# Optimization experiments

Hardware: AMD Instinct MI355X
Metric: run time of the kernel (lower is better)

Reference implementation:

```python
import jax, jax.numpy as jnp
import numpy as np

B, L, D, H, N = 1, 768, 128, 8, 6  # batch, seq len, model dim, heads, core_num
DH = D // H
EPS = 1e-5


def _layernorm(x, g, b):
    m = jnp.mean(x, axis=-1, keepdims=True)
    v = jnp.mean(jnp.square(x - m), axis=-1, keepdims=True)
    return (x - m) * jax.lax.rsqrt(v + EPS) * g + b


def setup_inputs() -> dict:
    key = jax.random.key(0)
    ks = jax.random.split(key, 12)
    s = 0.05

    def w(k, shape):
        return jax.random.normal(k, shape, dtype=jnp.float32) * s

    return {
        "x": jax.random.normal(ks[0], (B, L, D), dtype=jnp.float32),
        # JCrossOutProduct: l (in->mid), lo (mid->out); torch Linear convention y = x @ W.T + b
        "cop_l_w": w(ks[1], (N, D, D)), "cop_l_b": jnp.zeros((N, D), jnp.float32),
        "cop_lo_w": w(ks[2], (N, D, D)), "cop_lo_b": jnp.zeros((N, D), jnp.float32),
        # JResCOPAttn.l
        "cop_out_w": w(ks[3], (N, D, D)), "cop_out_b": jnp.zeros((N, D), jnp.float32),
        "cop_ln_g": jnp.ones((N, D), jnp.float32), "cop_ln_b": jnp.zeros((N, D), jnp.float32),
        # nn.MultiheadAttention: packed qkv in_proj + out_proj
        "qkv_w": w(ks[4], (N, 3 * D, D)), "qkv_b": jnp.zeros((N, 3 * D), jnp.float32),
        "mha_out_w": w(ks[5], (N, D, D)), "mha_out_b": jnp.zeros((N, D), jnp.float32),
        "mha_ln_g": jnp.ones((N, D), jnp.float32), "mha_ln_b": jnp.zeros((N, D), jnp.float32),
        # final l1
        "l1_w": w(ks[6], (D, D)), "l1_b": jnp.zeros((D,), jnp.float32),
    }


def reference(x, cop_l_w, cop_l_b, cop_lo_w, cop_lo_b, cop_out_w, cop_out_b,
              cop_ln_g, cop_ln_b, qkv_w, qkv_b, mha_out_w, mha_out_b,
              mha_ln_g, mha_ln_b, l1_w, l1_b):
    scale = 1.0 / np.sqrt(DH)
    for i in range(N):
        # ---- JResCOPAttn branch (AlphaFold-style outer product mean) ----
        a = x @ cop_l_w[i].T + cop_l_b[i]                          # [B,L,D]
        tm = jnp.einsum('bic,bjc->bijc', a, a)                     # [B,L,L,D] outer product
        tm = jnp.einsum('bijc,oc->bijo', tm, cop_lo_w[i]) + cop_lo_b[i]
        tx = x @ cop_out_w[i].T + cop_out_b[i]                     # [B,L,D]
        y1 = x + jnp.einsum('bijo,bjo->bio', tm, tx)               # '...cab,...ab->...cb'
        x1 = _layernorm(y1, cop_ln_g[i], cop_ln_b[i])              # dropout/act are identity
        # ---- JResSelfAttn branch (standard MHA, batch_first) ----
        qkv = x @ qkv_w[i].T + qkv_b[i]                            # [B,L,3D]
        q, k, v = jnp.split(qkv, 3, axis=-1)
        q = q.reshape(B, L, H, DH)
        k = k.reshape(B, L, H, DH)
        v = v.reshape(B, L, H, DH)
        scores = jnp.einsum('bihd,bjhd->bhij', q, k) * scale       # [B,H,L,L]
        attn = jax.nn.softmax(scores, axis=-1)
        o = jnp.einsum('bhij,bjhd->bihd', attn, v).reshape(B, L, D)
        y2 = x + (o @ mha_out_w[i].T + mha_out_b[i])
        x2 = _layernorm(y2, mha_ln_g[i], mha_ln_b[i])
        # ---- combine ----
        x = x + x1 + x2
    return x @ l1_w.T + l1_b
```

## Files before the change

kernel.cpp:

```cpp
#include <hip/hip_runtime.h>

#define L_SEQ 768
#define P_SZ  (L_SEQ * 128)

__device__ __forceinline__ unsigned short f2bf(float x) {
    unsigned int u = __float_as_uint(x);
    unsigned int r = (u + 0x7fffu + ((u >> 16) & 1u)) >> 16;
    return (unsigned short)r;
}

__device__ __forceinline__ void stage_x_tile(int tid, int r0, bool first,
    bool writeback, const float* xprev, const float* y1, const float* y2,
    const float* g1, const float* b1, const float* g2, const float* b2,
    float* xcur, float (*As)[132])
{
    const int row = tid >> 3;
    const int cs  = (tid & 7) * 16;
    const int gr  = (r0 + row) * 128 + cs;
    if (first) {
#pragma unroll
        for (int u = 0; u < 4; ++u)
            *(float4*)&As[row][cs + 4 * u] = *(const float4*)&xprev[gr + 4 * u];
        return;
    }
    float4 v1[4], v2[4];
    float s1 = 0.0f, s2 = 0.0f;
#pragma unroll
    for (int u = 0; u < 4; ++u) {
        v1[u] = *(const float4*)&y1[gr + 4 * u];
        v2[u] = *(const float4*)&y2[gr + 4 * u];
        s1 += v1[u].x + v1[u].y + v1[u].z + v1[u].w;
        s2 += v2[u].x + v2[u].y + v2[u].z + v2[u].w;
    }
#pragma unroll
    for (int m = 1; m < 8; m <<= 1) { s1 += __shfl_xor(s1, m); s2 += __shfl_xor(s2, m); }
    const float mu1 = s1 * (1.0f / 128.0f), mu2 = s2 * (1.0f / 128.0f);
    float q1 = 0.0f, q2 = 0.0f;
#pragma unroll
    for (int u = 0; u < 4; ++u) {
        float d;
        d = v1[u].x - mu1; q1 += d * d;  d = v1[u].y - mu1; q1 += d * d;
        d = v1[u].z - mu1; q1 += d * d;  d = v1[u].w - mu1; q1 += d * d;
        d = v2[u].x - mu2; q2 += d * d;  d = v2[u].y - mu2; q2 += d * d;
        d = v2[u].z - mu2; q2 += d * d;  d = v2[u].w - mu2; q2 += d * d;
    }
#pragma unroll
    for (int m = 1; m < 8; m <<= 1) { q1 += __shfl_xor(q1, m); q2 += __shfl_xor(q2, m); }
    const float rs1 = rsqrtf(q1 * (1.0f / 128.0f) + 1e-5f);
    const float rs2 = rsqrtf(q2 * (1.0f / 128.0f) + 1e-5f);
#pragma unroll
    for (int u = 0; u < 4; ++u) {
        float4 ga = *(const float4*)&g1[cs + 4 * u];
        float4 ba = *(const float4*)&b1[cs + 4 * u];
        float4 gb = *(const float4*)&g2[cs + 4 * u];
        float4 bb = *(const float4*)&b2[cs + 4 * u];
        float4 xv = *(const float4*)&xprev[gr + 4 * u];
        float4 o;
        o.x = xv.x + (v1[u].x - mu1) * rs1 * ga.x + ba.x + (v2[u].x - mu2) * rs2 * gb.x + bb.x;
        o.y = xv.y + (v1[u].y - mu1) * rs1 * ga.y + ba.y + (v2[u].y - mu2) * rs2 * gb.y + bb.y;
        o.z = xv.z + (v1[u].z - mu1) * rs1 * ga.z + ba.z + (v2[u].z - mu2) * rs2 * gb.z + bb.z;
        o.w = xv.w + (v1[u].w - mu1) * rs1 * ga.w + ba.w + (v2[u].w - mu2) * rs2 * gb.w + bb.w;
        *(float4*)&As[row][cs + 4 * u] = o;
        if (writeback) *(float4*)&xcur[gr + 4 * u] = o;
    }
}

__global__ __launch_bounds__(256) void megaK(int first,
    const float* __restrict__ xprev, const float* __restrict__ y1,
    const float* __restrict__ y2, float* __restrict__ xcur,
    const float* __restrict__ g1, const float* __restrict__ b1,
    const float* __restrict__ g2, const float* __restrict__ b2,
    const float* __restrict__ lw, const float* __restrict__ lb,
    const float* __restrict__ ow, const float* __restrict__ ob,
    const float* __restrict__ qw, const float* __restrict__ qb,
    float* __restrict__ a, float* __restrict__ tx, float* __restrict__ qkv)
{
    __shared__ float Bs[64][132];
    __shared__ float As[32][132];
    const int bid = blockIdx.x;
    const int tid = threadIdx.x;
    const int ct = bid / 24, rt = bid % 24;
    const int r0 = rt * 32;
    stage_x_tile(tid, r0, first != 0, (!first && ct == 0), xprev, y1, y2,
                 g1, b1, g2, b2, xcur, As);
    const float* W; const float* bias; float* outp; int ldC, colbase;
    if (ct < 2)      { W = lw; bias = lb; outp = a;   ldC = 128; colbase = ct * 64; }
    else if (ct < 4) { W = ow; bias = ob; outp = tx;  ldC = 128; colbase = (ct - 2) * 64; }
    else             { W = qw; bias = qb; outp = qkv; ldC = 384; colbase = (ct - 4) * 64; }
#pragma unroll
    for (int t = 0; t < 8; ++t) {
        int idx = tid + 256 * t;
        int brow = idx >> 5, f4 = idx & 31;
        *(float4*)&Bs[brow][f4 * 4] = *(const float4*)&W[(colbase + brow) * 128 + f4 * 4];
    }
    __syncthreads();
    const int rg = tid >> 4, ng = tid & 15;
    float accs[2][4];
#pragma unroll
    for (int c = 0; c < 4; ++c) {
        float bv = bias[colbase + ng + 16 * c];
        accs[0][c] = bv; accs[1][c] = bv;
    }
#pragma unroll 8
    for (int kk = 0; kk < 32; ++kk) {
        float4 a1 = *(const float4*)&As[rg][kk * 4];
        float4 a2 = *(const float4*)&As[rg + 16][kk * 4];
#pragma unroll
        for (int c = 0; c < 4; ++c) {
            float4 b = *(const float4*)&Bs[ng + 16 * c][kk * 4];
            accs[0][c] += a1.x * b.x + a1.y * b.y + a1.z * b.z + a1.w * b.w;
            accs[1][c] += a2.x * b.x + a2.y * b.y + a2.z * b.z + a2.w * b.w;
        }
    }
    const int r1 = r0 + rg, r2 = r0 + rg + 16;
#pragma unroll
    for (int c = 0; c < 4; ++c) {
        int gc = colbase + ng + 16 * c;
        outp[r1 * ldC + gc] = accs[0][c];
        outp[r2 * ldC + gc] = accs[1][c];
    }
}

__global__ __launch_bounds__(256) void k2K(const float* __restrict__ qkv,
    const float* __restrict__ a_, const float* __restrict__ tx_,
    float* __restrict__ o_, float* __restrict__ Mpart, float* __restrict__ tspart)
{
    __shared__ __align__(16) char smem[61440];
    const int bid = blockIdx.x;
    const int tid = threadIdx.x;
    if (bid < 192) {
        float* Ks = (float*)smem;
        float* Vs = Ks + 384 * 20;
        const int h = bid / 24;
        const int ch = bid % 24;
        const int base = ch * 32;
        const int lane = tid & 63;
        const int w = tid >> 6;
        const int p = lane & 31;
        const int rgidx = w * 2 + (lane >> 5);

        float q[4][16];
#pragma unroll
        for (int rr = 0; rr < 4; ++rr) {
            int r = base + rgidx * 4 + rr;
            const float4* qr = (const float4*)(qkv + r * 384 + h * 16);
#pragma unroll
            for (int s = 0; s < 4; ++s) {
                float4 v = qr[s];
                q[rr][s * 4 + 0] = v.x; q[rr][s * 4 + 1] = v.y;
                q[rr][s * 4 + 2] = v.z; q[rr][s * 4 + 3] = v.w;
            }
        }
        float m[4], l[4], acc[4][16];
#pragma unroll
        for (int rr = 0; rr < 4; ++rr) {
            m[rr] = -1e30f; l[rr] = 0.0f;
#pragma unroll
            for (int d = 0; d < 16; ++d) acc[rr][d] = 0.0f;
        }
        for (int ps = 0; ps < 2; ++ps) {
            __syncthreads();
#pragma unroll
            for (int t = 0; t < 6; ++t) {
                int idx = tid + 256 * t;
                int jj = idx >> 2, seg = idx & 3;
                int j = ps * 384 + jj;
                *(float4*)&Ks[jj * 20 + seg * 4] =
                    *(const float4*)&qkv[j * 384 + 128 + h * 16 + seg * 4];
                *(float4*)&Vs[jj * 20 + seg * 4] =
                    *(const float4*)&qkv[j * 384 + 256 + h * 16 + seg * 4];
            }
            __syncthreads();
            for (int jj2 = 0; jj2 < 12; ++jj2) {
                int jl = jj2 * 32 + p;
                float k16[16], v16[16];
#pragma unroll
                for (int s = 0; s < 4; ++s) {
                    float4 kv = *(const float4*)&Ks[jl * 20 + s * 4];
                    k16[s * 4 + 0] = kv.x; k16[s * 4 + 1] = kv.y;
                    k16[s * 4 + 2] = kv.z; k16[s * 4 + 3] = kv.w;
                    float4 vv = *(const float4*)&Vs[jl * 20 + s * 4];
                    v16[s * 4 + 0] = vv.x; v16[s * 4 + 1] = vv.y;
                    v16[s * 4 + 2] = vv.z; v16[s * 4 + 3] = vv.w;
                }
#pragma unroll
                for (int rr = 0; rr < 4; ++rr) {
                    float sc = 0.0f;
#pragma unroll
                    for (int d = 0; d < 16; ++d) sc += q[rr][d] * k16[d];
                    sc *= 0.25f;
                    if (sc > m[rr] + 8.0f) {
                        float f = __expf(m[rr] - sc);
                        l[rr] *= f;
#pragma unroll
                        for (int d = 0; d < 16; ++d) acc[rr][d] *= f;
                        m[rr] = sc;
                    }
                    float pe = __expf(sc - m[rr]);
                    l[rr] += pe;
#pragma unroll
                    for (int d = 0; d < 16; ++d) acc[rr][d] += pe * v16[d];
                }
            }
        }
        __syncthreads();
        float* sm = (float*)smem;
        float* sl = sm + 1024;
        unsigned short* sacc = (unsigned short*)(sl + 1024);
#pragma unroll
        for (int rr = 0; rr < 4; ++rr) {
            int row = rgidx * 4 + rr;
            sm[p * 32 + row] = m[rr];
            sl[p * 32 + row] = l[rr];
            unsigned int wbuf[8];
#pragma unroll
            for (int d2 = 0; d2 < 8; ++d2) {
                unsigned int lo = f2bf(acc[rr][2 * d2]);
                unsigned int hi = f2bf(acc[rr][2 * d2 + 1]);
                wbuf[d2] = lo | (hi << 16);
            }
            uint4* dst = (uint4*)&sacc[(p * 32 + row) * 24];
            dst[0] = make_uint4(wbuf[0], wbuf[1], wbuf[2], wbuf[3]);
            dst[1] = make_uint4(wbuf[4], wbuf[5], wbuf[6], wbuf[7]);
        }
        __syncthreads();
        {
            const int row = tid >> 3, dp = tid & 7;
            float M = -1e30f;
#pragma unroll
            for (int pp = 0; pp < 32; ++pp) M = fmaxf(M, sm[pp * 32 + row]);
            float L = 0.0f, o0 = 0.0f, o1 = 0.0f;
#pragma unroll
            for (int pp = 0; pp < 32; ++pp) {
                float f = __expf(sm[pp * 32 + row] - M);
                L += sl[pp * 32 + row] * f;
                unsigned int wv = *(const unsigned int*)&sacc[(pp * 32 + row) * 24 + 2 * dp];
                o0 += f * __uint_as_float(wv << 16);
                o1 += f * __uint_as_float(wv & 0xffff0000u);
            }
            float inv = 1.0f / L;
            *(float2*)&o_[(base + row) * 128 + h * 16 + 2 * dp] =
                make_float2(o0 * inv, o1 * inv);
        }
    } else {
        const int idx0 = bid - 192;
        const int jc = idx0 >> 2, ot = idx0 & 3;
        const int j0 = jc * 48;
        float* As  = (float*)smem;
        float* Ts  = As + 48 * 128;
        float* red = Ts + 48 * 32;
#pragma unroll
        for (int t = 0; t < 6; ++t) {
            int ix = tid + 256 * t;
            int jj = ix >> 5, f4 = ix & 31;
            *(float4*)&As[jj * 128 + f4 * 4] =
                *(const float4*)&a_[(j0 + jj) * 128 + f4 * 4];
        }
#pragma unroll
        for (int t = 0; t < 2; ++t) {
            int ix = tid + 256 * t;
            if (ix < 384) {
                int jj = ix >> 3, f4 = ix & 7;
                *(float4*)&Ts[jj * 32 + f4 * 4] =
                    *(const float4*)&tx_[(j0 + jj) * 128 + ot * 32 + f4 * 4];
            }
        }
        __syncthreads();
        const int c4 = tid & 31, owt = tid >> 5;
        float accm[4][4] = {};
#pragma unroll 4
        for (int jj = 0; jj < 48; ++jj) {
            float4 av = *(const float4*)&As[jj * 128 + c4 * 4];
            float4 tv = *(const float4*)&Ts[jj * 32 + owt * 4];
            float avv[4] = {av.x, av.y, av.z, av.w};
            float tvv[4] = {tv.x, tv.y, tv.z, tv.w};
#pragma unroll
            for (int oi = 0; oi < 4; ++oi)
#pragma unroll
                for (int ci = 0; ci < 4; ++ci)
                    accm[oi][ci] += avv[ci] * tvv[oi];
        }
#pragma unroll
        for (int oi = 0; oi < 4; ++oi) {
            *(float4*)&Mpart[jc * 16384 + (ot * 32 + owt * 4 + oi) * 128 + c4 * 4] =
                make_float4(accm[oi][0], accm[oi][1], accm[oi][2], accm[oi][3]);
        }
        {
            const int o = tid & 31, g = tid >> 5;
            float s = 0.0f;
#pragma unroll
            for (int jj = 0; jj < 6; ++jj) s += Ts[(g * 6 + jj) * 32 + o];
            red[g * 32 + o] = s;
        }
        __syncthreads();
        if (tid < 32) {
            float s = 0.0f;
#pragma unroll
            for (int g = 0; g < 8; ++g) s += red[g * 32 + tid];
            tspart[jc * 128 + ot * 32 + tid] = s;
        }
    }
}

__global__ __launch_bounds__(256) void ygemmK(
    const float* __restrict__ a_, const float* __restrict__ o_,
    const float* __restrict__ Mpart, const float* __restrict__ lo_w,
    const float* __restrict__ lob, const float* __restrict__ tspart,
    const float* __restrict__ mw, const float* __restrict__ mb,
    const float* __restrict__ xc, float* __restrict__ y1, float* __restrict__ y2)
{
    __shared__ float Bs[64][132];
    const int bid = blockIdx.x;
    const int tid = threadIdx.x;
    const int yb = bid / 24, rt = bid % 24;
    const float* A; float* C; int colbase;
    if (yb < 2) {
        colbase = yb * 64; A = a_; C = y1;
#pragma unroll
        for (int t = 0; t < 8; ++t) {
            int idx = tid + 256 * t;
            int row = idx >> 5, f4 = idx & 31;
            int o = colbase + row;
            float4 s = make_float4(0.f, 0.f, 0.f, 0.f);
#pragma unroll
            for (int jc = 0; jc < 16; ++jc) {
                float4 mv = *(const float4*)&Mpart[jc * 16384 + o * 128 + f4 * 4];
                s.x += mv.x; s.y += mv.y; s.z += mv.z; s.w += mv.w;
            }
            float4 lw4 = *(const float4*)&lo_w[o * 128 + f4 * 4];
            s.x *= lw4.x; s.y *= lw4.y; s.z *= lw4.z; s.w *= lw4.w;
            *(float4*)&Bs[row][f4 * 4] = s;
        }
    } else {
        colbase = (yb - 2) * 64; A = o_; C = y2;
#pragma unroll
        for (int t = 0; t < 8; ++t) {
            int idx = tid + 256 * t;
            int row = idx >> 5, f4 = idx & 31;
            *(float4*)&Bs[row][f4 * 4] =
                *(const float4*)&mw[(colbase + row) * 128 + f4 * 4];
        }
    }
    __syncthreads();
    const int rg = tid >> 4, ng = tid & 15;
    const int r0 = rt * 32;
    const int r1 = r0 + rg, r2 = r0 + rg + 16;
    float accs[2][4];
#pragma unroll
    for (int c = 0; c < 4; ++c) {
        int gc = colbase + ng + 16 * c;
        float bv;
        if (yb < 2) {
            float s = 0.0f;
#pragma unroll
            for (int jc = 0; jc < 16; ++jc) s += tspart[jc * 128 + gc];
            bv = lob[gc] * s;
        } else {
            bv = mb[gc];
        }
        accs[0][c] = bv; accs[1][c] = bv;
    }
    const float* A1 = A + r1 * 128;
    const float* A2 = A + r2 * 128;
#pragma unroll 8
    for (int kk = 0; kk < 32; ++kk) {
        float4 a1 = *(const float4*)&A1[kk * 4];
        float4 a2 = *(const float4*)&A2[kk * 4];
#pragma unroll
        for (int c = 0; c < 4; ++c) {
            float4 b = *(const float4*)&Bs[ng + 16 * c][kk * 4];
            accs[0][c] += a1.x * b.x + a1.y * b.y + a1.z * b.z + a1.w * b.w;
            accs[1][c] += a2.x * b.x + a2.y * b.y + a2.z * b.z + a2.w * b.w;
        }
    }
#pragma unroll
    for (int c = 0; c < 4; ++c) {
        int gc = colbase + ng + 16 * c;
        C[r1 * 128 + gc] = xc[r1 * 128 + gc] + accs[0][c];
        C[r2 * 128 + gc] = xc[r2 * 128 + gc] + accs[1][c];
    }
}

__global__ __launch_bounds__(256) void finK(
    const float* __restrict__ xprev, const float* __restrict__ y1,
    const float* __restrict__ y2,
    const float* __restrict__ g1, const float* __restrict__ b1,
    const float* __restrict__ g2, const float* __restrict__ b2,
    const float* __restrict__ w, const float* __restrict__ bias,
    float* __restrict__ outp)
{
    __shared__ float Bs[64][132];
    __shared__ float As[32][132];
    const int bid = blockIdx.x;
    const int tid = threadIdx.x;
    const int ct = bid / 24, rt = bid % 24;
    const int r0 = rt * 32;
    const int colbase = ct * 64;
    stage_x_tile(tid, r0, false, false, xprev, y1, y2, g1, b1, g2, b2,
                 nullptr, As);
#pragma unroll
    for (int t = 0; t < 8; ++t) {
        int idx = tid + 256 * t;
        int brow = idx >> 5, f4 = idx & 31;
        *(float4*)&Bs[brow][f4 * 4] = *(const float4*)&w[(colbase + brow) * 128 + f4 * 4];
    }
    __syncthreads();
    const int rg = tid >> 4, ng = tid & 15;
    float accs[2][4];
#pragma unroll
    for (int c = 0; c < 4; ++c) {
        float bv = bias[colbase + ng + 16 * c];
        accs[0][c] = bv; accs[1][c] = bv;
    }
#pragma unroll 8
    for (int kk = 0; kk < 32; ++kk) {
        float4 a1 = *(const float4*)&As[rg][kk * 4];
        float4 a2 = *(const float4*)&As[rg + 16][kk * 4];
#pragma unroll
        for (int c = 0; c < 4; ++c) {
            float4 b = *(const float4*)&Bs[ng + 16 * c][kk * 4];
            accs[0][c] += a1.x * b.x + a1.y * b.y + a1.z * b.z + a1.w * b.w;
            accs[1][c] += a2.x * b.x + a2.y * b.y + a2.z * b.z + a2.w * b.w;
        }
    }
    const int r1 = r0 + rg, r2 = r0 + rg + 16;
#pragma unroll
    for (int c = 0; c < 4; ++c) {
        int gc = colbase + ng + 16 * c;
        outp[r1 * 128 + gc] = accs[0][c];
        outp[r2 * 128 + gc] = accs[1][c];
    }
}

extern "C" void kernel_launch(void* const* d_in, const int* in_sizes, int n_in,
                              void* d_out, int out_size, void* d_ws, size_t ws_size,
                              hipStream_t stream)
{
    const float* x_in      = (const float*)d_in[0];
    const float* cop_l_w   = (const float*)d_in[1];
    const float* cop_l_b   = (const float*)d_in[2];
    const float* cop_lo_w  = (const float*)d_in[3];
    const float* cop_lo_b  = (const float*)d_in[4];
    const float* cop_out_w = (const float*)d_in[5];
    const float* cop_out_b = (const float*)d_in[6];
    const float* cop_ln_g  = (const float*)d_in[7];
    const float* cop_ln_b  = (const float*)d_in[8];
    const float* qkv_w     = (const float*)d_in[9];
    const float* qkv_b     = (const float*)d_in[10];
    const float* mha_out_w = (const float*)d_in[11];
    const float* mha_out_b = (const float*)d_in[12];
    const float* mha_ln_g  = (const float*)d_in[13];
    const float* mha_ln_b  = (const float*)d_in[14];
    const float* l1_w      = (const float*)d_in[15];
    const float* l1_b      = (const float*)d_in[16];

    float* ws = (float*)d_ws;
    float* xA     = ws + 0 * P_SZ;
    float* xB     = ws + 1 * P_SZ;
    float* a_     = ws + 2 * P_SZ;
    float* tx_    = ws + 3 * P_SZ;
    float* y1_    = ws + 4 * P_SZ;
    float* y2_    = ws + 5 * P_SZ;
    float* qkv_   = ws + 6 * P_SZ;
    float* o_     = ws + 9 * P_SZ;
    float* Mpart  = ws + 10 * P_SZ;
    float* tspart = Mpart + 16 * 16384;

    const float* xc = x_in;

    for (int i = 0; i < 6; ++i) {
        const float* lw  = cop_l_w   + i * 16384;
        const float* lb  = cop_l_b   + i * 128;
        const float* low = cop_lo_w  + i * 16384;
        const float* lob = cop_lo_b  + i * 128;
        const float* ow  = cop_out_w + i * 16384;
        const float* ob  = cop_out_b + i * 128;
        const float* qw  = qkv_w     + i * 49152;
        const float* qb  = qkv_b     + i * 384;
        const float* mw  = mha_out_w + i * 16384;
        const float* mb  = mha_out_b + i * 128;
        const float* pg1 = cop_ln_g + (i - 1) * 128;
        const float* pb1 = cop_ln_b + (i - 1) * 128;
        const float* pg2 = mha_ln_g + (i - 1) * 128;
        const float* pb2 = mha_ln_b + (i - 1) * 128;

        if (i == 0) {
            megaK<<<240, 256, 0, stream>>>(1, x_in, nullptr, nullptr, nullptr,
                                           nullptr, nullptr, nullptr, nullptr,
                                           lw, lb, ow, ob, qw, qb, a_, tx_, qkv_);
        } else {
            float* xn = (i & 1) ? xB : xA;
            megaK<<<240, 256, 0, stream>>>(0, xc, y1_, y2_, xn,
                                           pg1, pb1, pg2, pb2,
                                           lw, lb, ow, ob, qw, qb, a_, tx_, qkv_);
            xc = xn;
        }
        k2K<<<256, 256, 0, stream>>>(qkv_, a_, tx_, o_, Mpart, tspart);
        ygemmK<<<96, 256, 0, stream>>>(a_, o_, Mpart, low, lob, tspart, mw, mb,
                                       xc, y1_, y2_);
    }

    finK<<<48, 256, 0, stream>>>(xc, y1_, y2_,
                                 cop_ln_g + 5 * 128, cop_ln_b + 5 * 128,
                                 mha_ln_g + 5 * 128, mha_ln_b + 5 * 128,
                                 l1_w, l1_b, (float*)d_out);
}
```

Before: 284.4 us.

## Halve row tiles and restructure attention to raise block counts across kernels

Shrinks the row tile of the GEMM-style kernels (megaK, ygemmK, finK) from 32 to 16 rows, doubling grid sizes. The attention part of k2K is reworked so each thread handles one query row over a 12-key slice, with 16 partial softmax states merged through fp32 shared memory instead of bf16. The outer-product partial reduction now loops over two 48-row halves per block, halving the number of Mpart partials. The aim is more blocks and occupancy on a small problem, at the cost of less register reuse per thread and fewer keys processed per thread in attention.

```diff
diff --git a/kernel.cpp b/kernel.cpp
--- a/kernel.cpp
+++ b/kernel.cpp
@@ -3,41 +3,35 @@
 #define L_SEQ 768
 #define P_SZ  (L_SEQ * 128)
 
-__device__ __forceinline__ unsigned short f2bf(float x) {
-    unsigned int u = __float_as_uint(x);
-    unsigned int r = (u + 0x7fffu + ((u >> 16) & 1u)) >> 16;
-    return (unsigned short)r;
-}
-
-__device__ __forceinline__ void stage_x_tile(int tid, int r0, bool first,
+__device__ __forceinline__ void stage16(int tid, int r0, bool first,
     bool writeback, const float* xprev, const float* y1, const float* y2,
     const float* g1, const float* b1, const float* g2, const float* b2,
     float* xcur, float (*As)[132])
 {
-    const int row = tid >> 3;
-    const int cs  = (tid & 7) * 16;
+    const int row = tid >> 4;
+    const int cs  = (tid & 15) * 8;
     const int gr  = (r0 + row) * 128 + cs;
     if (first) {
 #pragma unroll
-        for (int u = 0; u < 4; ++u)
+        for (int u = 0; u < 2; ++u)
             *(float4*)&As[row][cs + 4 * u] = *(const float4*)&xprev[gr + 4 * u];
         return;
     }
-    float4 v1[4], v2[4];
+    float4 v1[2], v2[2];
     float s1 = 0.0f, s2 = 0.0f;
 #pragma unroll
-    for (int u = 0; u < 4; ++u) {
+    for (int u = 0; u < 2; ++u) {
         v1[u] = *(const float4*)&y1[gr + 4 * u];
         v2[u] = *(const float4*)&y2[gr + 4 * u];
         s1 += v1[u].x + v1[u].y + v1[u].z + v1[u].w;
         s2 += v2[u].x + v2[u].y + v2[u].z + v2[u].w;
     }
 #pragma unroll
-    for (int m = 1; m < 8; m <<= 1) { s1 += __shfl_xor(s1, m); s2 += __shfl_xor(s2, m); }
+    for (int m = 1; m < 16; m <<= 1) { s1 += __shfl_xor(s1, m); s2 += __shfl_xor(s2, m); }
     const float mu1 = s1 * (1.0f / 128.0f), mu2 = s2 * (1.0f / 128.0f);
     float q1 = 0.0f, q2 = 0.0f;
 #pragma unroll
-    for (int u = 0; u < 4; ++u) {
+    for (int u = 0; u < 2; ++u) {
         float d;
         d = v1[u].x - mu1; q1 += d * d;  d = v1[u].y - mu1; q1 += d * d;
         d = v1[u].z - mu1; q1 += d * d;  d = v1[u].w - mu1; q1 += d * d;
@@ -45,11 +39,11 @@
         d = v2[u].z - mu2; q2 += d * d;  d = v2[u].w - mu2; q2 += d * d;
     }
 #pragma unroll
-    for (int m = 1; m < 8; m <<= 1) { q1 += __shfl_xor(q1, m); q2 += __shfl_xor(q2, m); }
+    for (int m = 1; m < 16; m <<= 1) { q1 += __shfl_xor(q1, m); q2 += __shfl_xor(q2, m); }
     const float rs1 = rsqrtf(q1 * (1.0f / 128.0f) + 1e-5f);
     const float rs2 = rsqrtf(q2 * (1.0f / 128.0f) + 1e-5f);
 #pragma unroll
-    for (int u = 0; u < 4; ++u) {
+    for (int u = 0; u < 2; ++u) {
         float4 ga = *(const float4*)&g1[cs + 4 * u];
         float4 ba = *(const float4*)&b1[cs + 4 * u];
         float4 gb = *(const float4*)&g2[cs + 4 * u];
@@ -65,7 +59,7 @@
     }
 }
 
-__global__ __launch_bounds__(256) void megaK(int first,
+__global__ __launch_bounds__(256, 4) void megaK(int first,
     const float* __restrict__ xprev, const float* __restrict__ y1,
     const float* __restrict__ y2, float* __restrict__ xcur,
     const float* __restrict__ g1, const float* __restrict__ b1,
@@ -76,13 +70,13 @@
     float* __restrict__ a, float* __restrict__ tx, float* __restrict__ qkv)
 {
     __shared__ float Bs[64][132];
-    __shared__ float As[32][132];
+    __shared__ float As[16][132];
     const int bid = blockIdx.x;
     const int tid = threadIdx.x;
-    const int ct = bid / 24, rt = bid % 24;
-    const int r0 = rt * 32;
-    stage_x_tile(tid, r0, first != 0, (!first && ct == 0), xprev, y1, y2,
-                 g1, b1, g2, b2, xcur, As);
+    const int ct = bid / 48, rt = bid % 48;
+    const int r0 = rt * 16;
+    stage16(tid, r0, first != 0, (!first && ct == 0), xprev, y1, y2,
+            g1, b1, g2, b2, xcur, As);
     const float* W; const float* bias; float* outp; int ldC, colbase;
     if (ct < 2)      { W = lw; bias = lb; outp = a;   ldC = 128; colbase = ct * 64; }
     else if (ct < 4) { W = ow; bias = ob; outp = tx;  ldC = 128; colbase = (ct - 2) * 64; }
@@ -95,202 +89,170 @@
     }
     __syncthreads();
     const int rg = tid >> 4, ng = tid & 15;
-    float accs[2][4];
-#pragma unroll
-    for (int c = 0; c < 4; ++c) {
-        float bv = bias[colbase + ng + 16 * c];
-        accs[0][c] = bv; accs[1][c] = bv;
-    }
+    float accs[4];
+#pragma unroll
+    for (int c = 0; c < 4; ++c) accs[c] = bias[colbase + ng + 16 * c];
 #pragma unroll 8
     for (int kk = 0; kk < 32; ++kk) {
         float4 a1 = *(const float4*)&As[rg][kk * 4];
-        float4 a2 = *(const float4*)&As[rg + 16][kk * 4];
 #pragma unroll
         for (int c = 0; c < 4; ++c) {
             float4 b = *(const float4*)&Bs[ng + 16 * c][kk * 4];
-            accs[0][c] += a1.x * b.x + a1.y * b.y + a1.z * b.z + a1.w * b.w;
-            accs[1][c] += a2.x * b.x + a2.y * b.y + a2.z * b.z + a2.w * b.w;
-        }
-    }
-    const int r1 = r0 + rg, r2 = r0 + rg + 16;
-#pragma unroll
-    for (int c = 0; c < 4; ++c) {
-        int gc = colbase + ng + 16 * c;
-        outp[r1 * ldC + gc] = accs[0][c];
-        outp[r2 * ldC + gc] = accs[1][c];
-    }
-}
-
-__global__ __launch_bounds__(256) void k2K(const float* __restrict__ qkv,
+            accs[c] += a1.x * b.x + a1.y * b.y + a1.z * b.z + a1.w * b.w;
+        }
+    }
+    const int r = r0 + rg;
+#pragma unroll
+    for (int c = 0; c < 4; ++c)
+        outp[r * ldC + colbase + ng + 16 * c] = accs[c];
+}
+
+__global__ __launch_bounds__(256, 4) void k2K(const float* __restrict__ qkv,
     const float* __restrict__ a_, const float* __restrict__ tx_,
     float* __restrict__ o_, float* __restrict__ Mpart, float* __restrict__ tspart)
 {
-    __shared__ __align__(16) char smem[61440];
+    __shared__ __align__(16) char smem[49152];
     const int bid = blockIdx.x;
     const int tid = threadIdx.x;
-    if (bid < 192) {
+    if (bid < 384) {
         float* Ks = (float*)smem;
-        float* Vs = Ks + 384 * 20;
-        const int h = bid / 24;
-        const int ch = bid % 24;
-        const int base = ch * 32;
-        const int lane = tid & 63;
-        const int w = tid >> 6;
-        const int p = lane & 31;
-        const int rgidx = w * 2 + (lane >> 5);
-
-        float q[4][16];
-#pragma unroll
-        for (int rr = 0; rr < 4; ++rr) {
-            int r = base + rgidx * 4 + rr;
-            const float4* qr = (const float4*)(qkv + r * 384 + h * 16);
+        float* Vs = Ks + 192 * 20;
+        float* sm = Vs + 192 * 20;
+        float* sl = sm + 256;
+        float* sacc = sl + 256;
+        const int h = bid / 48;
+        const int ch = bid % 48;
+        const int r = tid & 15;
+        const int part = tid >> 4;
+        const int qi = ch * 16 + r;
+
+        float q[16];
+        {
+            const float4* qr = (const float4*)(qkv + qi * 384 + h * 16);
 #pragma unroll
             for (int s = 0; s < 4; ++s) {
                 float4 v = qr[s];
-                q[rr][s * 4 + 0] = v.x; q[rr][s * 4 + 1] = v.y;
-                q[rr][s * 4 + 2] = v.z; q[rr][s * 4 + 3] = v.w;
-            }
-        }
-        float m[4], l[4], acc[4][16];
-#pragma unroll
-        for (int rr = 0; rr < 4; ++rr) {
-            m[rr] = -1e30f; l[rr] = 0.0f;
-#pragma unroll
-            for (int d = 0; d < 16; ++d) acc[rr][d] = 0.0f;
-        }
-        for (int ps = 0; ps < 2; ++ps) {
+                q[s * 4 + 0] = v.x; q[s * 4 + 1] = v.y;
+                q[s * 4 + 2] = v.z; q[s * 4 + 3] = v.w;
+            }
+        }
+        float m = -1e30f, l = 0.0f;
+        float acc[16];
+#pragma unroll
+        for (int d = 0; d < 16; ++d) acc[d] = 0.0f;
+
+        for (int s = 0; s < 4; ++s) {
             __syncthreads();
 #pragma unroll
-            for (int t = 0; t < 6; ++t) {
+            for (int t = 0; t < 3; ++t) {
                 int idx = tid + 256 * t;
-                int jj = idx >> 2, seg = idx & 3;
-                int j = ps * 384 + jj;
-                *(float4*)&Ks[jj * 20 + seg * 4] =
-                    *(const float4*)&qkv[j * 384 + 128 + h * 16 + seg * 4];
-                *(float4*)&Vs[jj * 20 + seg * 4] =
-                    *(const float4*)&qkv[j * 384 + 256 + h * 16 + seg * 4];
+                int row = idx >> 2, d4 = idx & 3;
+                int j = s * 192 + row;
+                *(float4*)&Ks[row * 20 + d4 * 4] =
+                    *(const float4*)&qkv[j * 384 + 128 + h * 16 + d4 * 4];
+                *(float4*)&Vs[row * 20 + d4 * 4] =
+                    *(const float4*)&qkv[j * 384 + 256 + h * 16 + d4 * 4];
             }
             __syncthreads();
-            for (int jj2 = 0; jj2 < 12; ++jj2) {
-                int jl = jj2 * 32 + p;
-                float k16[16], v16[16];
-#pragma unroll
-                for (int s = 0; s < 4; ++s) {
-                    float4 kv = *(const float4*)&Ks[jl * 20 + s * 4];
-                    k16[s * 4 + 0] = kv.x; k16[s * 4 + 1] = kv.y;
-                    k16[s * 4 + 2] = kv.z; k16[s * 4 + 3] = kv.w;
-                    float4 vv = *(const float4*)&Vs[jl * 20 + s * 4];
-                    v16[s * 4 + 0] = vv.x; v16[s * 4 + 1] = vv.y;
-                    v16[s * 4 + 2] = vv.z; v16[s * 4 + 3] = vv.w;
+            const int tb = part * 12;
+            for (int jj = 0; jj < 12; ++jj) {
+                int t = tb + jj;
+                float sc = 0.0f;
+#pragma unroll
+                for (int d = 0; d < 16; ++d) sc += q[d] * Ks[t * 20 + d];
+                sc *= 0.25f;
+                float p;
+                if (sc > m) {
+                    float f = __expf(m - sc);
+                    l *= f;
+#pragma unroll
+                    for (int d = 0; d < 16; ++d) acc[d] *= f;
+                    m = sc;
+                    p = 1.0f;
+                } else {
+                    p = __expf(sc - m);
                 }
-#pragma unroll
-                for (int rr = 0; rr < 4; ++rr) {
-                    float sc = 0.0f;
-#pragma unroll
-                    for (int d = 0; d < 16; ++d) sc += q[rr][d] * k16[d];
-                    sc *= 0.25f;
-                    if (sc > m[rr] + 8.0f) {
-                        float f = __expf(m[rr] - sc);
-                        l[rr] *= f;
-#pragma unroll
-                        for (int d = 0; d < 16; ++d) acc[rr][d] *= f;
-                        m[rr] = sc;
-                    }
-                    float pe = __expf(sc - m[rr]);
-                    l[rr] += pe;
-#pragma unroll
-                    for (int d = 0; d < 16; ++d) acc[rr][d] += pe * v16[d];
-                }
-            }
-        }
+                l += p;
+#pragma unroll
+                for (int d = 0; d < 16; ++d) acc[d] += p * Vs[t * 20 + d];
+            }
+        }
+        sm[part * 16 + r] = m;
+        sl[part * 16 + r] = l;
+#pragma unroll
+        for (int d = 0; d < 16; ++d) sacc[(part * 16 + r) * 16 + d] = acc[d];
         __syncthreads();
-        float* sm = (float*)smem;
-        float* sl = sm + 1024;
-        unsigned short* sacc = (unsigned short*)(sl + 1024);
-#pragma unroll
-        for (int rr = 0; rr < 4; ++rr) {
-            int row = rgidx * 4 + rr;
-            sm[p * 32 + row] = m[rr];
-            sl[p * 32 + row] = l[rr];
-            unsigned int wbuf[8];
-#pragma unroll
-            for (int d2 = 0; d2 < 8; ++d2) {
-                unsigned int lo = f2bf(acc[rr][2 * d2]);
-                unsigned int hi = f2bf(acc[rr][2 * d2 + 1]);
-                wbuf[d2] = lo | (hi << 16);
-            }
-            uint4* dst = (uint4*)&sacc[(p * 32 + row) * 24];
-            dst[0] = make_uint4(wbuf[0], wbuf[1], wbuf[2], wbuf[3]);
-            dst[1] = make_uint4(wbuf[4], wbuf[5], wbuf[6], wbuf[7]);
-        }
-        __syncthreads();
-        {
-            const int row = tid >> 3, dp = tid & 7;
-            float M = -1e30f;
-#pragma unroll
-            for (int pp = 0; pp < 32; ++pp) M = fmaxf(M, sm[pp * 32 + row]);
-            float L = 0.0f, o0 = 0.0f, o1 = 0.0f;
-#pragma unroll
-            for (int pp = 0; pp < 32; ++pp) {
-                float f = __expf(sm[pp * 32 + row] - M);
-                L += sl[pp * 32 + row] * f;
-                unsigned int wv = *(const unsigned int*)&sacc[(pp * 32 + row) * 24 + 2 * dp];
-                o0 += f * __uint_as_float(wv << 16);
-                o1 += f * __uint_as_float(wv & 0xffff0000u);
-            }
-            float inv = 1.0f / L;
-            *(float2*)&o_[(base + row) * 128 + h * 16 + 2 * dp] =
-                make_float2(o0 * inv, o1 * inv);
-        }
+
+        const int row = tid >> 4, d = tid & 15;
+        float M = sm[row];
+#pragma unroll
+        for (int p = 1; p < 16; ++p) M = fmaxf(M, sm[p * 16 + row]);
+        float L = 0.0f, o = 0.0f;
+#pragma unroll
+        for (int p = 0; p < 16; ++p) {
+            float f = __expf(sm[p * 16 + row] - M);
+            L += sl[p * 16 + row] * f;
+            o += sacc[(p * 16 + row) * 16 + d] * f;
+        }
+        o_[(ch * 16 + row) * 128 + h * 16 + d] = o / L;
     } else {
-        const int idx0 = bid - 192;
+        const int idx0 = bid - 384;
         const int jc = idx0 >> 2, ot = idx0 & 3;
-        const int j0 = jc * 48;
         float* As  = (float*)smem;
         float* Ts  = As + 48 * 128;
         float* red = Ts + 48 * 32;
-#pragma unroll
-        for (int t = 0; t < 6; ++t) {
-            int ix = tid + 256 * t;
-            int jj = ix >> 5, f4 = ix & 31;
-            *(float4*)&As[jj * 128 + f4 * 4] =
-                *(const float4*)&a_[(j0 + jj) * 128 + f4 * 4];
-        }
-#pragma unroll
-        for (int t = 0; t < 2; ++t) {
-            int ix = tid + 256 * t;
-            if (ix < 384) {
-                int jj = ix >> 3, f4 = ix & 7;
-                *(float4*)&Ts[jj * 32 + f4 * 4] =
-                    *(const float4*)&tx_[(j0 + jj) * 128 + ot * 32 + f4 * 4];
-            }
-        }
-        __syncthreads();
         const int c4 = tid & 31, owt = tid >> 5;
         float accm[4][4] = {};
+        float tsacc = 0.0f;
+        for (int half = 0; half < 2; ++half) {
+            const int j0 = jc * 96 + half * 48;
+            __syncthreads();
+#pragma unroll
+            for (int t = 0; t < 6; ++t) {
+                int ix = tid + 256 * t;
+                int jj = ix >> 5, f4 = ix & 31;
+                *(float4*)&As[jj * 128 + f4 * 4] =
+                    *(const float4*)&a_[(j0 + jj) * 128 + f4 * 4];
+            }
+#pragma unroll
+            for (int t = 0; t < 2; ++t) {
+                int ix = tid + 256 * t;
+                if (ix < 384) {
+                    int jj = ix >> 3, f4 = ix & 7;
+                    *(float4*)&Ts[jj * 32 + f4 * 4] =
+                        *(const float4*)&tx_[(j0 + jj) * 128 + ot * 32 + f4 * 4];
+                }
+            }
+            __syncthreads();
 #pragma unroll 4
-        for (int jj = 0; jj < 48; ++jj) {
-            float4 av = *(const float4*)&As[jj * 128 + c4 * 4];
-            float4 tv = *(const float4*)&Ts[jj * 32 + owt * 4];
-            float avv[4] = {av.x, av.y, av.z, av.w};
-            float tvv[4] = {tv.x, tv.y, tv.z, tv.w};
-#pragma unroll
-            for (int oi = 0; oi < 4; ++oi)
-#pragma unroll
-                for (int ci = 0; ci < 4; ++ci)
-                    accm[oi][ci] += avv[ci] * tvv[oi];
+            for (int jj = 0; jj < 48; ++jj) {
+                float4 av = *(const float4*)&As[jj * 128 + c4 * 4];
+                float4 tv = *(const float4*)&Ts[jj * 32 + owt * 4];
+                float avv[4] = {av.x, av.y, av.z, av.w};
+                float tvv[4] = {tv.x, tv.y, tv.z, tv.w};
+#pragma unroll
+                for (int oi = 0; oi < 4; ++oi)
+#pragma unroll
+                    for (int ci = 0; ci < 4; ++ci)
+                        accm[oi][ci] += avv[ci] * tvv[oi];
+            }
+            {
+                const int o = tid & 31, g = tid >> 5;
+                float s = 0.0f;
+#pragma unroll
+                for (int jj = 0; jj < 6; ++jj) s += Ts[(g * 6 + jj) * 32 + o];
+                tsacc += s;
+            }
         }
 #pragma unroll
         for (int oi = 0; oi < 4; ++oi) {
             *(float4*)&Mpart[jc * 16384 + (ot * 32 + owt * 4 + oi) * 128 + c4 * 4] =
                 make_float4(accm[oi][0], accm[oi][1], accm[oi][2], accm[oi][3]);
         }
+        __syncthreads();
         {
             const int o = tid & 31, g = tid >> 5;
-            float s = 0.0f;
-#pragma unroll
-            for (int jj = 0; jj < 6; ++jj) s += Ts[(g * 6 + jj) * 32 + o];
-            red[g * 32 + o] = s;
+            red[g * 32 + o] = tsacc;
         }
         __syncthreads();
         if (tid < 32) {
@@ -302,7 +264,7 @@
     }
 }
 
-__global__ __launch_bounds__(256) void ygemmK(
+__global__ __launch_bounds__(256, 4) void ygemmK(
     const float* __restrict__ a_, const float* __restrict__ o_,
     const float* __restrict__ Mpart, const float* __restrict__ lo_w,
     const float* __restrict__ lob, const float* __restrict__ tspart,
@@ -312,7 +274,7 @@
     __shared__ float Bs[64][132];
     const int bid = blockIdx.x;
     const int tid = threadIdx.x;
-    const int yb = bid / 24, rt = bid % 24;
+    const int yb = bid / 48, rt = bid % 48;
     const float* A; float* C; int colbase;
     if (yb < 2) {
         colbase = yb * 64; A = a_; C = y1;
@@ -323,7 +285,7 @@
             int o = colbase + row;
             float4 s = make_float4(0.f, 0.f, 0.f, 0.f);
 #pragma unroll
-            for (int jc = 0; jc < 16; ++jc) {
+            for (int jc = 0; jc < 8; ++jc) {
                 float4 mv = *(const float4*)&Mpart[jc * 16384 + o * 128 + f4 * 4];
                 s.x += mv.x; s.y += mv.y; s.z += mv.z; s.w += mv.w;
             }
@@ -343,9 +305,8 @@
     }
     __syncthreads();
     const int rg = tid >> 4, ng = tid & 15;
-    const int r0 = rt * 32;
-    const int r1 = r0 + rg, r2 = r0 + rg + 16;
-    float accs[2][4];
+    const int r = rt * 16 + rg;
+    float accs[4];
 #pragma unroll
     for (int c = 0; c < 4; ++c) {
         int gc = colbase + ng + 16 * c;
@@ -353,35 +314,31 @@
         if (yb < 2) {
             float s = 0.0f;
 #pragma unroll
-            for (int jc = 0; jc < 16; ++jc) s += tspart[jc * 128 + gc];
+            for (int jc = 0; jc < 8; ++jc) s += tspart[jc * 128 + gc];
             bv = lob[gc] * s;
         } else {
             bv = mb[gc];
         }
-        accs[0][c] = bv; accs[1][c] = bv;
-    }
-    const float* A1 = A + r1 * 128;
-    const float* A2 = A + r2 * 128;
+        accs[c] = bv;
+    }
+    const float* A1 = A + r * 128;
 #pragma unroll 8
     for (int kk = 0; kk < 32; ++kk) {
         float4 a1 = *(const float4*)&A1[kk * 4];
-        float4 a2 = *(const float4*)&A2[kk * 4];
 #pragma unroll
         for (int c = 0; c < 4; ++c) {
             float4 b = *(const float4*)&Bs[ng + 16 * c][kk * 4];
-            accs[0][c] += a1.x * b.x + a1.y * b.y + a1.z * b.z + a1.w * b.w;
-            accs[1][c] += a2.x * b.x + a2.y * b.y + a2.z * b.z + a2.w * b.w;
+            accs[c] += a1.x * b.x + a1.y * b.y + a1.z * b.z + a1.w * b.w;
         }
     }
 #pragma unroll
     for (int c = 0; c < 4; ++c) {
         int gc = colbase + ng + 16 * c;
-        C[r1 * 128 + gc] = xc[r1 * 128 + gc] + accs[0][c];
-        C[r2 * 128 + gc] = xc[r2 * 128 + gc] + accs[1][c];
-    }
-}
-
-__global__ __launch_bounds__(256) void finK(
+        C[r * 128 + gc] = xc[r * 128 + gc] + accs[c];
+    }
+}
+
+__global__ __launch_bounds__(256, 4) void finK(
     const float* __restrict__ xprev, const float* __restrict__ y1,
     const float* __restrict__ y2,
     const float* __restrict__ g1, const float* __restrict__ b1,
@@ -390,14 +347,13 @@
     float* __restrict__ outp)
 {
     __shared__ float Bs[64][132];
-    __shared__ float As[32][132];
+    __shared__ float As[16][132];
     const int bid = blockIdx.x;
     const int tid = threadIdx.x;
-    const int ct = bid / 24, rt = bid % 24;
-    const int r0 = rt * 32;
+    const int ct = bid / 48, rt = bid % 48;
+    const int r0 = rt * 16;
     const int colbase = ct * 64;
-    stage_x_tile(tid, r0, false, false, xprev, y1, y2, g1, b1, g2, b2,
-                 nullptr, As);
+    stage16(tid, r0, false, false, xprev, y1, y2, g1, b1, g2, b2, nullptr, As);
 #pragma unroll
     for (int t = 0; t < 8; ++t) {
         int idx = tid + 256 * t;
@@ -406,30 +362,22 @@
     }
     __syncthreads();
     const int rg = tid >> 4, ng = tid & 15;
-    float accs[2][4];
-#pragma unroll
-    for (int c = 0; c < 4; ++c) {
-        float bv = bias[colbase + ng + 16 * c];
-        accs[0][c] = bv; accs[1][c] = bv;
-    }
+    float accs[4];
+#pragma unroll
+    for (int c = 0; c < 4; ++c) accs[c] = bias[colbase + ng + 16 * c];
 #pragma unroll 8
     for (int kk = 0; kk < 32; ++kk) {
         float4 a1 = *(const float4*)&As[rg][kk * 4];
-        float4 a2 = *(const float4*)&As[rg + 16][kk * 4];
 #pragma unroll
         for (int c = 0; c < 4; ++c) {
             float4 b = *(const float4*)&Bs[ng + 16 * c][kk * 4];
-            accs[0][c] += a1.x * b.x + a1.y * b.y + a1.z * b.z + a1.w * b.w;
-            accs[1][c] += a2.x * b.x + a2.y * b.y + a2.z * b.z + a2.w * b.w;
-        }
-    }
-    const int r1 = r0 + rg, r2 = r0 + rg + 16;
-#pragma unroll
-    for (int c = 0; c < 4; ++c) {
-        int gc = colbase + ng + 16 * c;
-        outp[r1 * 128 + gc] = accs[0][c];
-        outp[r2 * 128 + gc] = accs[1][c];
-    }
+            accs[c] += a1.x * b.x + a1.y * b.y + a1.z * b.z + a1.w * b.w;
+        }
+    }
+    const int r = r0 + rg;
+#pragma unroll
+    for (int c = 0; c < 4; ++c)
+        outp[r * 128 + colbase + ng + 16 * c] = accs[c];
 }
 
 extern "C" void kernel_launch(void* const* d_in, const int* in_sizes, int n_in,
@@ -464,7 +412,7 @@
     float* qkv_   = ws + 6 * P_SZ;
     float* o_     = ws + 9 * P_SZ;
     float* Mpart  = ws + 10 * P_SZ;
-    float* tspart = Mpart + 16 * 16384;
+    float* tspart = Mpart + 8 * 16384;
 
     const float* xc = x_in;
 
@@ -485,22 +433,22 @@
         const float* pb2 = mha_ln_b + (i - 1) * 128;
 
         if (i == 0) {
-            megaK<<<240, 256, 0, stream>>>(1, x_in, nullptr, nullptr, nullptr,
+            megaK<<<480, 256, 0, stream>>>(1, x_in, nullptr, nullptr, nullptr,
                                            nullptr, nullptr, nullptr, nullptr,
                                            lw, lb, ow, ob, qw, qb, a_, tx_, qkv_);
         } else {
             float* xn = (i & 1) ? xB : xA;
-            megaK<<<240, 256, 0, stream>>>(0, xc, y1_, y2_, xn,
+            megaK<<<480, 256, 0, stream>>>(0, xc, y1_, y2_, xn,
                                            pg1, pb1, pg2, pb2,
                                            lw, lb, ow, ob, qw, qb, a_, tx_, qkv_);
             xc = xn;
         }
-        k2K<<<256, 256, 0, stream>>>(qkv_, a_, tx_, o_, Mpart, tspart);
-        ygemmK<<<96, 256, 0, stream>>>(a_, o_, Mpart, low, lob, tspart, mw, mb,
-                                       xc, y1_, y2_);
-    }
-
-    finK<<<48, 256, 0, stream>>>(xc, y1_, y2_,
+        k2K<<<416, 256, 0, stream>>>(qkv_, a_, tx_, o_, Mpart, tspart);
+        ygemmK<<<192, 256, 0, stream>>>(a_, o_, Mpart, low, lob, tspart, mw, mb,
+                                        xc, y1_, y2_);
+    }
+
+    finK<<<96, 256, 0, stream>>>(xc, y1_, y2_,
                                  cop_ln_g + 5 * 128, cop_ln_b + 5 * 128,
                                  mha_ln_g + 5 * 128, mha_ln_b + 5 * 128,
                                  l1_w, l1_b, (float*)d_out);
```

After: 258.1 us, median of 2. 9.3% less time.
